# Performance work log

Hardware: AMD Instinct MI355X
Metric: run time of the kernel (lower is better)

The kernel has to match this reference:

```python
import jax, jax.numpy as jnp
import numpy as np

B, T, C, O = 32, 2048, 1152, 29  # batch, temporal len, in channels (sum(data_length)), classes


def setup_inputs() -> dict:
    key = jax.random.key(0)
    k1, k2, k3, k4 = jax.random.split(key, 4)
    x = jax.random.normal(k1, (B, T, C), dtype=jnp.float32)
    # per-sample valid length, >=1 to avoid div-by-zero
    length = jax.random.randint(k2, (B,), 1, T + 1, dtype=jnp.int64)
    # Conv1d(C, O, 1) weight [O, C, 1] -> stored as [O, C]; bias [O]
    W = jax.random.normal(k3, (O, C), dtype=jnp.float32) * (1.0 / np.sqrt(C))
    b = jax.random.normal(k4, (O,), dtype=jnp.float32) * 0.01
    return {"x": x, "length": length, "W": W, "b": b}


def reference(x, length, W, b):
    # x: [B, T, C]; scale/shift then 1x1 conv (pointwise linear) then sum over T.
    # Linearity lets us fuse: sum_t (W @ (x/64 - 2) + b) == einsum + T*b.
    y = x / 64.0 - 2.0                      # [B, T, C]
    z = jnp.einsum('btc,oc->bo', y, W)      # temporal-summed projection [B, O]
    z = z + jnp.asarray(x.shape[1], z.dtype) * b
    return z / length.astype(z.dtype)[:, None]
```

## Files before the change

### kernel.cpp

```cpp
#include <hip/hip_runtime.h>


#define PB 32
#define PT 2048
#define PC 1152
#define PO 29
#define TSPLIT 32
#define ROWS (PT / TSPLIT)
#define C4 (PC / 4)

__global__ __launch_bounds__(288) void sum_slab_kernel(const float* __restrict__ x,
                                                       float* __restrict__ sp) {
    const int b   = blockIdx.x;
    const int p   = blockIdx.y;
    const int tid = threadIdx.x;

    const float4* __restrict__ src =
        (const float4*)x + ((size_t)b * PT + (size_t)p * ROWS) * C4 + tid;

    float4 acc = make_float4(0.f, 0.f, 0.f, 0.f);

#pragma unroll 8
    for (int t = 0; t < ROWS; ++t) {
        float4 v = src[(size_t)t * C4];
        acc.x += v.x; acc.y += v.y; acc.z += v.z; acc.w += v.w;
    }

    float4* __restrict__ dst = (float4*)sp + ((size_t)b * TSPLIT + p) * C4 + tid;
    *dst = acc;
}

__global__ __launch_bounds__(256) void finish_kernel(const float* __restrict__ sp,
                                                     const float* __restrict__ W,
                                                     const float* __restrict__ bias,
                                                     const int* __restrict__ length,
                                                     float* __restrict__ out) {
    const int b   = blockIdx.x;
    const int tid = threadIdx.x;

    __shared__ float s_hat[PC];

    const float4* __restrict__ spb = (const float4*)sp + (size_t)b * TSPLIT * C4;

    for (int c4 = tid; c4 < C4; c4 += 256) {
        float4 a = make_float4(0.f, 0.f, 0.f, 0.f);
#pragma unroll 8
        for (int p = 0; p < TSPLIT; ++p) {
            float4 v = spb[(size_t)p * C4 + c4];
            a.x += v.x; a.y += v.y; a.z += v.z; a.w += v.w;
        }
        const float scale = 1.0f / 64.0f;
        const float shift = -2.0f * (float)PT;
        s_hat[c4 * 4 + 0] = a.x * scale + shift;
        s_hat[c4 * 4 + 1] = a.y * scale + shift;
        s_hat[c4 * 4 + 2] = a.z * scale + shift;
        s_hat[c4 * 4 + 3] = a.w * scale + shift;
    }
    __syncthreads();

    const int wave = tid >> 6;
    const int lane = tid & 63;
    const float inv_len = 1.0f / (float)length[b];

    for (int o = wave; o < PO; o += 4) {
        const float* __restrict__ Wo = W + (size_t)o * PC;
        float dot = 0.f;
#pragma unroll
        for (int c = lane; c < PC; c += 64) {
            dot += Wo[c] * s_hat[c];
        }
#pragma unroll
        for (int off = 32; off > 0; off >>= 1) {
            dot += __shfl_down(dot, off);
        }
        if (lane == 0) {
            out[b * PO + o] = (dot + (float)PT * bias[o]) * inv_len;
        }
    }
}

extern "C" void kernel_launch(void* const* d_in, const int* in_sizes, int n_in,
                              void* d_out, int out_size, void* d_ws, size_t ws_size,
                              hipStream_t stream) {
    const float* x      = (const float*)d_in[0];
    const int*   length = (const int*)d_in[1];
    const float* W      = (const float*)d_in[2];
    const float* bias   = (const float*)d_in[3];
    float*       out    = (float*)d_out;
    float*       sp     = (float*)d_ws;

    dim3 g1(PB, TSPLIT);
    sum_slab_kernel<<<g1, C4, 0, stream>>>(x, sp);

    finish_kernel<<<PB, 256, 0, stream>>>(sp, W, bias, length, out);
}
```

Baseline: 457.5 us.

## Fuse per-slab projection into slab kernel and shrink the partial-sum reduction

Each block now sums a 128-row slab using 576 threads in two phases, merges the two halves through shared memory, and projects the slab sum onto W directly. Only 29 partial dot products per slab go to the workspace, not 1152 channel sums. The second kernel then only adds 16 small partials per output. This removes the heavy partial-sum write and re-read and halves the number of slab blocks, at the cost of re-reading W (small, cache-resident) in every block and some extra shared-memory work.

```diff
diff --git a/kernel.cpp b/kernel.cpp
--- a/kernel.cpp
+++ b/kernel.cpp
@@ -5,77 +5,86 @@
 #define PT 2048
 #define PC 1152
 #define PO 29
-#define TSPLIT 32
-#define ROWS (PT / TSPLIT)
+#define NS 16
+#define SROWS (PT / NS)
 #define C4 (PC / 4)
+#define BT 576
+#define PASSES (SROWS / 2)
 
-__global__ __launch_bounds__(288) void sum_slab_kernel(const float* __restrict__ x,
-                                                       float* __restrict__ sp) {
+__global__ __launch_bounds__(BT) void slab_project_kernel(
+    const float* __restrict__ x,
+    const float* __restrict__ W,
+    float* __restrict__ zp)
+{
     const int b   = blockIdx.x;
-    const int p   = blockIdx.y;
+    const int s   = blockIdx.y;
     const int tid = threadIdx.x;
 
     const float4* __restrict__ src =
-        (const float4*)x + ((size_t)b * PT + (size_t)p * ROWS) * C4 + tid;
+        (const float4*)x + ((size_t)b * PT + (size_t)s * SROWS) * C4 + tid;
 
     float4 acc = make_float4(0.f, 0.f, 0.f, 0.f);
-
 #pragma unroll 8
-    for (int t = 0; t < ROWS; ++t) {
-        float4 v = src[(size_t)t * C4];
+    for (int t = 0; t < PASSES; ++t) {
+        float4 v = src[(size_t)t * BT];
         acc.x += v.x; acc.y += v.y; acc.z += v.z; acc.w += v.w;
     }
 
-    float4* __restrict__ dst = (float4*)sp + ((size_t)b * TSPLIT + p) * C4 + tid;
-    *dst = acc;
-}
+    __shared__ float lds[2 * PC];
+    {
+        const int phase = tid / C4;
+        const int c4    = tid % C4;
+        float4* l4 = (float4*)(lds + phase * PC) + c4;
+        *l4 = acc;
+    }
+    __syncthreads();
 
-__global__ __launch_bounds__(256) void finish_kernel(const float* __restrict__ sp,
-                                                     const float* __restrict__ W,
-                                                     const float* __restrict__ bias,
-                                                     const int* __restrict__ length,
-                                                     float* __restrict__ out) {
-    const int b   = blockIdx.x;
-    const int tid = threadIdx.x;
-
-    __shared__ float s_hat[PC];
-
-    const float4* __restrict__ spb = (const float4*)sp + (size_t)b * TSPLIT * C4;
-
-    for (int c4 = tid; c4 < C4; c4 += 256) {
-        float4 a = make_float4(0.f, 0.f, 0.f, 0.f);
-#pragma unroll 8
-        for (int p = 0; p < TSPLIT; ++p) {
-            float4 v = spb[(size_t)p * C4 + c4];
-            a.x += v.x; a.y += v.y; a.z += v.z; a.w += v.w;
-        }
+    {
         const float scale = 1.0f / 64.0f;
-        const float shift = -2.0f * (float)PT;
-        s_hat[c4 * 4 + 0] = a.x * scale + shift;
-        s_hat[c4 * 4 + 1] = a.y * scale + shift;
-        s_hat[c4 * 4 + 2] = a.z * scale + shift;
-        s_hat[c4 * 4 + 3] = a.w * scale + shift;
+        const float shift = -2.0f * (float)SROWS;
+        const int c0 = tid;
+        const int c1 = tid + BT;
+        float v0 = (lds[c0] + lds[PC + c0]) * scale + shift;
+        float v1 = (lds[c1] + lds[PC + c1]) * scale + shift;
+        lds[c0] = v0;
+        lds[c1] = v1;
     }
     __syncthreads();
 
     const int wave = tid >> 6;
     const int lane = tid & 63;
-    const float inv_len = 1.0f / (float)length[b];
-
-    for (int o = wave; o < PO; o += 4) {
+    for (int o = wave; o < PO; o += 9) {
         const float* __restrict__ Wo = W + (size_t)o * PC;
         float dot = 0.f;
 #pragma unroll
         for (int c = lane; c < PC; c += 64) {
-            dot += Wo[c] * s_hat[c];
+            dot += Wo[c] * lds[c];
         }
 #pragma unroll
         for (int off = 32; off > 0; off >>= 1) {
             dot += __shfl_down(dot, off);
         }
         if (lane == 0) {
-            out[b * PO + o] = (dot + (float)PT * bias[o]) * inv_len;
+            zp[((size_t)b * NS + s) * PO + o] = dot;
         }
+    }
+}
+
+__global__ __launch_bounds__(64) void reduce_kernel(
+    const float* __restrict__ zp,
+    const float* __restrict__ bias,
+    const int*  __restrict__ length,
+    float* __restrict__ out)
+{
+    const int b = blockIdx.x;
+    const int o = threadIdx.x;
+    if (o < PO) {
+        float acc = 0.f;
+#pragma unroll
+        for (int s = 0; s < NS; ++s) {
+            acc += zp[((size_t)b * NS + s) * PO + o];
+        }
+        out[b * PO + o] = (acc + (float)PT * bias[o]) / (float)length[b];
     }
 }
 
@@ -87,10 +96,10 @@
     const float* W      = (const float*)d_in[2];
     const float* bias   = (const float*)d_in[3];
     float*       out    = (float*)d_out;
-    float*       sp     = (float*)d_ws;
+    float*       zp     = (float*)d_ws;
 
-    dim3 g1(PB, TSPLIT);
-    sum_slab_kernel<<<g1, C4, 0, stream>>>(x, sp);
+    dim3 g1(PB, NS);
+    slab_project_kernel<<<g1, BT, 0, stream>>>(x, W, zp);
 
-    finish_kernel<<<PB, 256, 0, stream>>>(sp, W, bias, length, out);
+    reduce_kernel<<<PB, 64, 0, stream>>>(zp, bias, length, out);
 }
```

After: 419.7 us. 1.09x faster.
